# Optimization experiments

Hardware: AMD Instinct MI355X
Metric: run time of the kernel (lower is better)

## Reference

```python
import jax, jax.numpy as jnp
import numpy as np

N_EMBD = 1024
H_DIM = 1024
NB = 16          # blocks resolved by _find_dynamic_num_blocks for all projections
N_MEM = 128
N_FORG = H_DIM - N_MEM
RANK = 64
LOG_DT_INIT = -2.0
EPS = 1.1920929e-07  # torch fp32 finfo eps used by F.rms_norm


def rms_norm(x):
    return x * jax.lax.rsqrt(jnp.mean(jnp.square(x), axis=-1, keepdims=True) + EPS)


def silu(x):
    return x * jax.nn.sigmoid(x)


def blockdiag(x, w):
    # x: [..., nb*bi], w: [nb, bo, bi] -> [..., nb*bo]
    nb, bo, bi = w.shape
    xs = x.reshape(*x.shape[:-1], nb, bi)
    y = jnp.einsum('...ni,noi->...no', xs, w)
    return y.reshape(*x.shape[:-1], nb * bo)


def causal_scan(drive, a):
    # drive: [B,T,D] float32, a: [D] per-channel decay; causal conv with kernel a^t via FFT
    B, T, D = drive.shape
    steps = jnp.arange(T, dtype=jnp.float32)
    kernel = jnp.exp(jnp.log(jnp.maximum(a, 1e-6))[:, None] * steps[None, :])  # [D,T]
    n_fft = 1 << int(2 * T - 1).bit_length()
    df = jnp.fft.rfft(drive.astype(jnp.float32).transpose(0, 2, 1), n=n_fft, axis=-1)
    kf = jnp.fft.rfft(kernel, n=n_fft, axis=-1)
    y = jnp.fft.irfft(df * kf[None], n=n_fft, axis=-1)[..., :T]
    return y.transpose(0, 2, 1).astype(drive.dtype)


def geom_gain(a, K):
    one_minus = 1.0 - a
    safe = jnp.maximum(one_minus, 1e-8)
    return jnp.where(jnp.abs(one_minus) < 1e-6,
                     jnp.full_like(a, float(K)),
                     (1.0 - a ** K) / safe)


def setup_inputs() -> dict:
    key = jax.random.key(0)
    ks = jax.random.split(key, 10)
    s = 0.02
    bi_e, bo_h = N_EMBD // NB, H_DIM // NB
    bi_p = (2 * N_EMBD + H_DIM) // NB
    bo_e = N_EMBD // NB
    return {
        'x': jax.random.normal(ks[0], (4, 4096, N_EMBD), dtype=jnp.float32),
        'active_k': 4,
        'b_seq_w': jax.random.normal(ks[1], (NB, bo_h, bi_e), jnp.float32) * s,
        'b_depth_w': jax.random.normal(ks[2], (NB, bo_h, bi_e), jnp.float32) * s,
        'w_post_w': jax.random.normal(ks[3], (NB, bo_h, bi_p), jnp.float32) * s,
        'w_local_w': jax.random.normal(ks[4], (NB, bo_e, H_DIM // NB), jnp.float32) * s,
        'lr_A': jax.random.normal(ks[5], (N_EMBD, RANK), jnp.float32) * s,
        'lr_B': jax.random.normal(ks[6], (RANK, H_DIM), jnp.float32) * s,
        'log_A_seq': jnp.zeros((H_DIM,), jnp.float32),
        'log_dt_seq': jnp.full((H_DIM,), LOG_DT_INIT, jnp.float32),
        'log_A_depth': jnp.zeros((N_FORG,), jnp.float32),
        'log_dt_depth': jnp.full((N_FORG,), LOG_DT_INIT, jnp.float32),
    }


def reference(x, active_k, b_seq_w, b_depth_w, w_post_w, w_local_w, lr_A, lr_B,
              log_A_seq, log_dt_seq, log_A_depth, log_dt_depth):
    K = int(active_k)
    e = rms_norm(x)
    shifted_e = jnp.pad(e[:, :-1], ((0, 0), (1, 0), (0, 0)))
    a_seq = jnp.exp(-jnp.exp(log_A_seq) * jnp.exp(log_dt_seq))
    h_seq = causal_scan(silu(blockdiag(e, b_seq_w)), a_seq)
    a_forg = jnp.exp(-jnp.exp(log_A_depth) * jnp.exp(log_dt_depth))
    a_depth = jnp.concatenate([jnp.ones((N_MEM,), a_forg.dtype), a_forg], axis=0)
    gain = geom_gain(a_depth, K).astype(x.dtype)
    h_depth = gain * silu(blockdiag(e, b_depth_w))
    h = h_seq + h_depth
    r = silu(blockdiag(jnp.concatenate([rms_norm(h), e, shifted_e], axis=-1), w_post_w))
    out = x + blockdiag(r, w_local_w) + (r @ lr_B.T) @ lr_A.T
    return out
```

## Files before the change

### kernel.cpp

```cpp
#include <hip/hip_runtime.h>

#define B_ 4
#define T_ 4096
#define D_ 1024
#define R_ (B_*T_)
#define CHUNK_ 64
#define NCH_ (T_/CHUNK_)
#define EPS_ 1.1920929e-07f

typedef unsigned short ushort_t;
typedef __attribute__((ext_vector_type(8))) short short8;
typedef __attribute__((ext_vector_type(4))) float f32x4;

__device__ __forceinline__ float silu_f(float v){ return v / (1.0f + __expf(-v)); }

__device__ __forceinline__ ushort_t f2bf(float f){
    unsigned u = __float_as_uint(f);
    unsigned r = u + 0x7fffu + ((u>>16)&1u);
    return (ushort_t)(r>>16);
}
__device__ __forceinline__ float bf2f(ushort_t s){ return __uint_as_float(((unsigned)s)<<16); }

__device__ __forceinline__ f32x4 mfma16(short8 a, short8 b, f32x4 c){
    return __builtin_amdgcn_mfma_f32_16x16x32_bf16(a, b, c, 0, 0, 0);
}

__global__ void prep_k(const float* __restrict__ s0, const float* __restrict__ s1,
                       const float* __restrict__ s2, const float* __restrict__ s3,
                       const float* __restrict__ s4, const float* __restrict__ s5,
                       ushort_t* __restrict__ d0, ushort_t* __restrict__ d1,
                       ushort_t* __restrict__ d2, ushort_t* __restrict__ d3,
                       ushort_t* __restrict__ d4, ushort_t* __restrict__ d5,
                       const float* __restrict__ logA_seq, const float* __restrict__ logdt_seq,
                       const float* __restrict__ logA_dep, const float* __restrict__ logdt_dep,
                       const int* __restrict__ active_k,
                       float* __restrict__ aseq, float* __restrict__ apowC,
                       float* __restrict__ gain, float* __restrict__ apowtab){
    int i = blockIdx.x*256 + threadIdx.x;
    if      (i < 65536)   d0[i] = f2bf(s0[i]);
    else if (i < 131072)  d1[i-65536] = f2bf(s1[i-65536]);
    else if (i < 327680)  d2[i-131072] = f2bf(s2[i-131072]);
    else if (i < 393216)  d3[i-327680] = f2bf(s3[i-327680]);
    else if (i < 458752)  d4[i-393216] = f2bf(s4[i-393216]);
    else if (i < 524288)  d5[i-458752] = f2bf(s5[i-458752]);
    else if (i < 524288 + D_){
        int d = i - 524288;
        float K = (float)(*active_k);
        float a = expf(-expf(logA_seq[d]) * expf(logdt_seq[d]));
        a = fmaxf(a, 1e-6f);
        aseq[d] = a;
        apowC[d] = powf(a, (float)CHUNK_);
        float ap = a;
        for (int s2=0;s2<CHUNK_;++s2){ apowtab[s2*D_ + d] = ap; ap *= a; }
        float g;
        if (d < 128) {
            g = K;
        } else {
            float ad = expf(-expf(logA_dep[d-128]) * expf(logdt_dep[d-128]));
            float om = 1.0f - ad;
            if (fabsf(om) < 1e-6f) g = K;
            else g = (1.0f - powf(ad, K)) / fmaxf(om, 1e-8f);
        }
        gain[d] = g;
    }
}

__global__ __launch_bounds__(256) void rmsbf_k(const float* __restrict__ x, ushort_t* __restrict__ e){
    int row = blockIdx.x;
    int tid = threadIdx.x;
    float4 v = ((const float4*)(x + (size_t)row*D_))[tid];
    float ss = v.x*v.x + v.y*v.y + v.z*v.z + v.w*v.w;
    for (int off=32; off; off>>=1) ss += __shfl_down(ss, off, 64);
    __shared__ float red[4];
    if ((tid&63)==0) red[tid>>6] = ss;
    __syncthreads();
    float tot = red[0]+red[1]+red[2]+red[3];
    float scale = 1.0f / sqrtf(tot*(1.0f/D_) + EPS_);
    ushort4 o;
    o.x = f2bf(v.x*scale); o.y = f2bf(v.y*scale); o.z = f2bf(v.z*scale); o.w = f2bf(v.w*scale);
    ((ushort4*)(e + (size_t)row*D_))[tid] = o;
}

__global__ __launch_bounds__(256) void bd2s_k(const ushort_t* __restrict__ e,
        const ushort_t* __restrict__ wseq, const ushort_t* __restrict__ wdep,
        const float* __restrict__ gain, const float* __restrict__ aseq,
        ushort_t* __restrict__ hsum, float* __restrict__ carry){
    __shared__ __align__(16) ushort_t sd[4][16][72];
    __shared__ __align__(16) ushort_t sh[4][16][72];
    int wave = threadIdx.x>>6, lane = threadIdx.x&63;
    int m = lane&15, quad = lane>>4;
    int orow = lane>>2, oq = lane&3;
    int n = blockIdx.y;
    int chunk0 = blockIdx.x*256 + wave*64;

    short8 bs[2][4], bd[2][4];
    #pragma unroll
    for (int s=0;s<2;++s)
        #pragma unroll
        for (int c=0;c<4;++c){
            bs[s][c] = *(const short8*)(wseq + n*4096 + (c*16+m)*64 + s*32 + quad*8);
            bd[s][c] = *(const short8*)(wdep + n*4096 + (c*16+m)*64 + s*32 + quad*8);
        }
    float g[4];
    #pragma unroll
    for (int c=0;c<4;++c) g[c] = gain[n*64 + c*16 + m];

    float a = aseq[n*64 + lane];
    float hh = 0.f;

    #pragma unroll
    for (int t=0;t<4;++t){
        int r0 = chunk0 + t*16;
        const ushort_t* ab = e + (size_t)(r0+m)*D_ + n*64 + quad*8;
        short8 a0 = *(const short8*)ab;
        short8 a1 = *(const short8*)(ab + 32);
        f32x4 accs[4], accd[4];
        #pragma unroll
        for (int c=0;c<4;++c){
            accs[c]=(f32x4)0.f; accd[c]=(f32x4)0.f;
            accs[c]=mfma16(a0, bs[0][c], accs[c]);
            accd[c]=mfma16(a0, bd[0][c], accd[c]);
            accs[c]=mfma16(a1, bs[1][c], accs[c]);
            accd[c]=mfma16(a1, bd[1][c], accd[c]);
        }
        #pragma unroll
        for (int c=0;c<4;++c)
            #pragma unroll
            for (int r=0;r<4;++r){
                sd[wave][quad*4+r][c*16+m] = f2bf(silu_f(accs[c][r]));
                sh[wave][quad*4+r][c*16+m] = f2bf(g[c]*silu_f(accd[c][r]));
            }
        #pragma unroll
        for (int s=0;s<16;++s){
            hh = fmaf(a, hh, bf2f(sd[wave][s][lane]));
            sd[wave][s][lane] = f2bf(hh + bf2f(sh[wave][s][lane]));
        }
        ushort_t* db = hsum + (size_t)(r0+orow)*D_ + n*64;
        #pragma unroll
        for (int it=0;it<2;++it)
            *(short8*)(db + (it*4+oq)*8) = *(const short8*)&sd[wave][orow][(it*4+oq)*8];
    }
    carry[(size_t)(chunk0>>6)*D_ + n*64 + lane] = hh;
}

__global__ __launch_bounds__(256) void scan2_k(float* __restrict__ carry, const float* __restrict__ apowC){
    int tid = blockIdx.x*256 + threadIdx.x;
    int d = tid & (D_-1);
    int b = tid >> 10;
    float aC = apowC[d];
    float pref = 0.f;
    for (int c=0;c<NCH_;++c){
        size_t idx = (size_t)(b*NCH_+c)*D_ + d;
        float s = carry[idx];
        carry[idx] = pref;
        pref = fmaf(aC, pref, s);
    }
}

__global__ __launch_bounds__(256) void scan3s_k(const ushort_t* __restrict__ hsum,
                                                const float* __restrict__ aseq,
                                                const float* __restrict__ carry,
                                                const float* __restrict__ apowtab,
                                                ushort_t* __restrict__ hn){
    __shared__ float part[4][4];
    __shared__ float scl[8];
    int tid = threadIdx.x;
    int lane = tid & 63, wave = tid >> 6;
    int cg = tid & 127;
    int rp = tid >> 7;
    int d0 = cg*8;
    int row0 = blockIdx.x*8;
    int bc = row0 >> 6;
    int s0 = row0 & 63;

    float a2[8], P[8], apow[8];
    #pragma unroll
    for (int j=0;j<8;++j){
        float aj = aseq[d0+j];
        a2[j] = aj*aj;
        P[j]  = carry[(size_t)bc*D_ + d0 + j];
        apow[j] = apowtab[(size_t)(s0 + rp)*D_ + d0 + j];
    }

    float hf[4][8];
    #pragma unroll
    for (int i=0;i<4;++i){
        int row = row0 + i*2 + rp;
        short8 v = *(const short8*)(hsum + (size_t)row*D_ + d0);
        float ss = 0.f;
        #pragma unroll
        for (int j=0;j<8;++j){
            float f = bf2f((ushort_t)v[j]) + P[j]*apow[j];
            hf[i][j] = f;
            ss += f*f;
            apow[j] *= a2[j];
        }
        for (int off=32; off; off>>=1) ss += __shfl_down(ss, off, 64);
        if (lane==0) part[wave][i] = ss;
    }
    __syncthreads();
    if (tid < 8){
        int r = tid;
        int rr = r & 1, ii = r >> 1;
        float sum = part[rr*2][ii] + part[rr*2+1][ii];
        scl[r] = rsqrtf(sum*(1.0f/D_) + EPS_);
    }
    __syncthreads();
    #pragma unroll
    for (int i=0;i<4;++i){
        int rloc = i*2 + rp;
        float sc = scl[rloc];
        short8 o;
        #pragma unroll
        for (int j=0;j<8;++j) o[j] = (short)f2bf(hf[i][j]*sc);
        *(short8*)(hn + (size_t)(row0 + rloc)*D_ + d0) = o;
    }
}

__global__ __launch_bounds__(256) void post_k(const ushort_t* __restrict__ hn,
                                              const ushort_t* __restrict__ e,
                                              const ushort_t* __restrict__ wpost, ushort_t* __restrict__ rout){
    __shared__ __align__(16) ushort_t st[4][16][72];
    int wave = threadIdx.x>>6, lane = threadIdx.x&63;
    int m = lane&15, quad = lane>>4;
    int orow = lane>>2, oq = lane&3;
    int n = blockIdx.y;
    int row0 = blockIdx.x*128 + wave*32 + m;

    f32x4 acc[2][4];
    #pragma unroll
    for (int t=0;t<2;++t)
        #pragma unroll
        for (int c=0;c<4;++c) acc[t][c]=(f32x4)0.f;

    #pragma unroll 1
    for (int s=0;s<6;++s){
        int g0 = n*192 + s*32;
        short8 bw[4];
        #pragma unroll
        for (int c=0;c<4;++c)
            bw[c] = *(const short8*)(wpost + n*(64*192) + (c*16+m)*192 + s*32 + quad*8);
        #pragma unroll
        for (int t=0;t<2;++t){
            int row = row0 + t*16;
            short8 af;
            if (g0 < 1024){
                af = *(const short8*)(hn + (size_t)row*D_ + g0 + quad*8);
            } else if (g0 < 2048){
                af = *(const short8*)(e + (size_t)row*D_ + (g0-1024) + quad*8);
            } else {
                if ((row & (T_-1)) == 0) af = short8{0,0,0,0,0,0,0,0};
                else af = *(const short8*)(e + (size_t)(row-1)*D_ + (g0-2048) + quad*8);
            }
            #pragma unroll
            for (int c=0;c<4;++c)
                acc[t][c] = mfma16(af, bw[c], acc[t][c]);
        }
    }
    #pragma unroll
    for (int t=0;t<2;++t){
        int r0 = blockIdx.x*128 + wave*32 + t*16;
        #pragma unroll
        for (int c=0;c<4;++c)
            #pragma unroll
            for (int r=0;r<4;++r)
                st[wave][quad*4+r][c*16+m] = f2bf(silu_f(acc[t][c][r]));
        ushort_t* db = rout + (size_t)(r0+orow)*D_ + n*64;
        #pragma unroll
        for (int it=0;it<2;++it)
            *(short8*)(db + (it*4+oq)*8) = *(const short8*)&st[wave][orow][(it*4+oq)*8];
    }
}

__global__ __launch_bounds__(256) void rlow_k(const ushort_t* __restrict__ r, const ushort_t* __restrict__ lrB,
                                              ushort_t* __restrict__ rlow){
    __shared__ __align__(16) float sacc[4][16][68];
    int wave = threadIdx.x>>6, lane = threadIdx.x&63;
    int m = lane&15, quad = lane>>4;
    int r0 = blockIdx.x*16;
    f32x4 acc[4];
    #pragma unroll
    for (int c=0;c<4;++c) acc[c]=(f32x4)0.f;
    const ushort_t* ab = r + (size_t)(r0+m)*D_ + wave*256 + quad*8;
    #pragma unroll
    for (int s=0;s<8;++s){
        short8 a = *(const short8*)(ab + s*32);
        #pragma unroll
        for (int c=0;c<4;++c){
            short8 b = *(const short8*)(lrB + (c*16+m)*1024 + wave*256 + s*32 + quad*8);
            acc[c] = mfma16(a, b, acc[c]);
        }
    }
    #pragma unroll
    for (int c=0;c<4;++c)
        #pragma unroll
        for (int r2=0;r2<4;++r2)
            sacc[wave][quad*4+r2][c*16+m] = acc[c][r2];
    __syncthreads();
    int row  = threadIdx.x>>4;
    int col4 = (threadIdx.x&15)*4;
    float4 v0 = *(const float4*)&sacc[0][row][col4];
    float4 v1 = *(const float4*)&sacc[1][row][col4];
    float4 v2 = *(const float4*)&sacc[2][row][col4];
    float4 v3 = *(const float4*)&sacc[3][row][col4];
    ushort4 o;
    o.x = f2bf(v0.x+v1.x+v2.x+v3.x);
    o.y = f2bf(v0.y+v1.y+v2.y+v3.y);
    o.z = f2bf(v0.z+v1.z+v2.z+v3.z);
    o.w = f2bf(v0.w+v1.w+v2.w+v3.w);
    *(ushort4*)(rlow + (size_t)(r0+row)*64 + col4) = o;
}

__global__ __launch_bounds__(256) void out_k(const float* __restrict__ x, const ushort_t* __restrict__ r,
        const ushort_t* __restrict__ rlow, const ushort_t* __restrict__ wloc, const ushort_t* __restrict__ lrA,
        float* __restrict__ out){
    __shared__ __align__(16) float st[4][16][68];
    int wave = threadIdx.x>>6, lane = threadIdx.x&63;
    int m = lane&15, quad = lane>>4;
    int orow = lane>>2, oq = lane&3;
    int n = blockIdx.y;

    short8 wl[2][4], la[4][2];
    #pragma unroll
    for (int c=0;c<4;++c)
        #pragma unroll
        for (int s=0;s<2;++s){
            wl[s][c] = *(const short8*)(wloc + n*4096 + (c*16+m)*64 + s*32 + quad*8);
            la[c][s] = *(const short8*)(lrA + (size_t)(n*64 + c*16 + m)*64 + s*32 + quad*8);
        }
    #pragma unroll
    for (int t=0;t<2;++t){
        int r0 = blockIdx.x*128 + wave*32 + t*16;
        const float* xb = x + (size_t)(r0+orow)*D_ + n*64;
        float4 xv[4];
        #pragma unroll
        for (int it=0;it<4;++it) xv[it] = *(const float4*)(xb + (it*4+oq)*4);

        const ushort_t* lb = rlow + (size_t)(r0+m)*64 + quad*8;
        short8 al0 = *(const short8*)lb;
        short8 al1 = *(const short8*)(lb + 32);
        const ushort_t* ab = r + (size_t)(r0+m)*D_ + n*64 + quad*8;
        short8 ar0 = *(const short8*)ab;
        short8 ar1 = *(const short8*)(ab + 32);
        f32x4 acc[4];
        #pragma unroll
        for (int c=0;c<4;++c){
            acc[c]=(f32x4)0.f;
            acc[c]=mfma16(al0, la[c][0], acc[c]);
            acc[c]=mfma16(al1, la[c][1], acc[c]);
            acc[c]=mfma16(ar0, wl[0][c], acc[c]);
            acc[c]=mfma16(ar1, wl[1][c], acc[c]);
        }
        #pragma unroll
        for (int c=0;c<4;++c)
            #pragma unroll
            for (int r2=0;r2<4;++r2)
                st[wave][quad*4+r2][c*16+m] = acc[c][r2];
        float* ob = out + (size_t)(r0+orow)*D_ + n*64;
        #pragma unroll
        for (int it=0;it<4;++it){
            float4 v = *(const float4*)&st[wave][orow][(it*4+oq)*4];
            v.x += xv[it].x; v.y += xv[it].y; v.z += xv[it].z; v.w += xv[it].w;
            *(float4*)(ob + (it*4+oq)*4) = v;
        }
    }
}

extern "C" void kernel_launch(void* const* d_in, const int* in_sizes, int n_in,
                              void* d_out, int out_size, void* d_ws, size_t ws_size,
                              hipStream_t stream) {
    const float* x         = (const float*)d_in[0];
    const int*   active_k  = (const int*)  d_in[1];
    const float* b_seq_w   = (const float*)d_in[2];
    const float* b_depth_w = (const float*)d_in[3];
    const float* w_post_w  = (const float*)d_in[4];
    const float* w_local_w = (const float*)d_in[5];
    const float* lr_A      = (const float*)d_in[6];
    const float* lr_B      = (const float*)d_in[7];
    const float* logA_seq  = (const float*)d_in[8];
    const float* logdt_seq = (const float*)d_in[9];
    const float* logA_dep  = (const float*)d_in[10];
    const float* logdt_dep = (const float*)d_in[11];

    float* ws      = (float*)d_ws;
    float* carry   = ws;
    float* aseq    = carry + (size_t)B_*NCH_*D_;
    float* apowC   = aseq + D_;
    float* gain    = apowC + D_;
    float* apowtab = gain + D_;
    ushort_t* ub       = (ushort_t*)(apowtab + (size_t)CHUNK_*D_);
    ushort_t* e_bf     = ub;
    ushort_t* hsum_bf  = e_bf + (size_t)R_*D_;
    ushort_t* hn_bf    = hsum_bf + (size_t)R_*D_;
    ushort_t* r_bf     = hn_bf + (size_t)R_*D_;
    ushort_t* rlow_bf  = r_bf + (size_t)R_*D_;
    ushort_t* wseq_bf  = rlow_bf + (size_t)R_*64;
    ushort_t* wdep_bf  = wseq_bf + 65536;
    ushort_t* wpost_bf = wdep_bf + 65536;
    ushort_t* wloc_bf  = wpost_bf + 196608;
    ushort_t* lrA_bf   = wloc_bf + 65536;
    ushort_t* lrB_bf   = lrA_bf + 65536;

    prep_k<<<(524288 + D_ + 255)/256, 256, 0, stream>>>(
        b_seq_w, b_depth_w, w_post_w, w_local_w, lr_A, lr_B,
        wseq_bf, wdep_bf, wpost_bf, wloc_bf, lrA_bf, lrB_bf,
        logA_seq, logdt_seq, logA_dep, logdt_dep, active_k, aseq, apowC, gain, apowtab);

    rmsbf_k <<<R_, 256, 0, stream>>>(x, e_bf);
    bd2s_k  <<<dim3(R_/256, 16), 256, 0, stream>>>(e_bf, wseq_bf, wdep_bf, gain, aseq,
                                                   hsum_bf, carry);
    scan2_k <<<(B_*D_)/256, 256, 0, stream>>>(carry, apowC);
    scan3s_k<<<R_/8, 256, 0, stream>>>(hsum_bf, aseq, carry, apowtab, hn_bf);
    post_k  <<<dim3(R_/128, 16), 256, 0, stream>>>(hn_bf, e_bf, wpost_bf, r_bf);
    rlow_k  <<<R_/16, 256, 0, stream>>>(r_bf, lrB_bf, rlow_bf);
    out_k   <<<dim3(R_/128, 16), 256, 0, stream>>>(x, r_bf, rlow_bf, wloc_bf, lrA_bf, (float*)d_out);
}
```

Baseline: 271.6 us.

## Parallelize intra-chunk scan with lane shuffles; widen scan2 and out_k grids

The in-chunk linear recurrence in bd2s_k used to run as a serial 16-step loop through shared memory per 16-row tile. It is now a register-level parallel scan: each lane scans its 4 rows locally, and the lanes then combine (decay, offset) pairs across quads with __shfl_up. This also removes the second shared-memory buffer and keeps the scan state in fp32 rather than rounding to bf16 between steps, so numerics change slightly. Separately, scan2_k uses 64-thread blocks and loads all chunk carries into registers up front, and out_k handles one 16-row tile per wave over twice as many blocks, giving more parallelism.

```diff
diff --git a/kernel.cpp b/kernel.cpp
--- a/kernel.cpp
+++ b/kernel.cpp
@@ -85,8 +85,7 @@
         const ushort_t* __restrict__ wseq, const ushort_t* __restrict__ wdep,
         const float* __restrict__ gain, const float* __restrict__ aseq,
         ushort_t* __restrict__ hsum, float* __restrict__ carry){
-    __shared__ __align__(16) ushort_t sd[4][16][72];
-    __shared__ __align__(16) ushort_t sh[4][16][72];
+    __shared__ __align__(16) ushort_t st[4][16][72];
     int wave = threadIdx.x>>6, lane = threadIdx.x&63;
     int m = lane&15, quad = lane>>4;
     int orow = lane>>2, oq = lane&3;
@@ -101,12 +100,16 @@
             bs[s][c] = *(const short8*)(wseq + n*4096 + (c*16+m)*64 + s*32 + quad*8);
             bd[s][c] = *(const short8*)(wdep + n*4096 + (c*16+m)*64 + s*32 + quad*8);
         }
-    float g[4];
-    #pragma unroll
-    for (int c=0;c<4;++c) g[c] = gain[n*64 + c*16 + m];
-
-    float a = aseq[n*64 + lane];
-    float hh = 0.f;
+    float g[4], av[4], a4v[4], C[4];
+    #pragma unroll
+    for (int c=0;c<4;++c){
+        g[c]  = gain[n*64 + c*16 + m];
+        float a = aseq[n*64 + c*16 + m];
+        av[c] = a;
+        float a2 = a*a;
+        a4v[c] = a2*a2;
+        C[c] = 0.f;
+    }
 
     #pragma unroll
     for (int t=0;t<4;++t){
@@ -124,36 +127,59 @@
             accd[c]=mfma16(a1, bd[1][c], accd[c]);
         }
         #pragma unroll
-        for (int c=0;c<4;++c)
-            #pragma unroll
-            for (int r=0;r<4;++r){
-                sd[wave][quad*4+r][c*16+m] = f2bf(silu_f(accs[c][r]));
-                sh[wave][quad*4+r][c*16+m] = f2bf(g[c]*silu_f(accd[c][r]));
-            }
-        #pragma unroll
-        for (int s=0;s<16;++s){
-            hh = fmaf(a, hh, bf2f(sd[wave][s][lane]));
-            sd[wave][s][lane] = f2bf(hh + bf2f(sh[wave][s][lane]));
+        for (int c=0;c<4;++c){
+            float a  = av[c];
+            float d0 = silu_f(accs[c][0]);
+            float d1 = silu_f(accs[c][1]);
+            float d2 = silu_f(accs[c][2]);
+            float d3 = silu_f(accs[c][3]);
+            float p1 = fmaf(a, d0, d1);
+            float p2 = fmaf(a, p1, d2);
+            float p3 = fmaf(a, p2, d3);
+            float M = a4v[c], Bv = p3;
+            float Mp = __shfl_up(M, 16, 64);
+            float Bp = __shfl_up(Bv, 16, 64);
+            if (quad >= 1){ Bv = fmaf(M, Bp, Bv); M *= Mp; }
+            Mp = __shfl_up(M, 32, 64);
+            Bp = __shfl_up(Bv, 32, 64);
+            if (quad >= 2){ Bv = fmaf(M, Bp, Bv); M *= Mp; }
+            float KB = __shfl_up(Bv, 16, 64);
+            float KM = __shfl_up(M, 16, 64);
+            float K  = (quad==0) ? C[c] : fmaf(KM, C[c], KB);
+            float h0 = fmaf(a, K,  d0);
+            float h1 = fmaf(a, h0, d1);
+            float h2 = fmaf(a, h1, d2);
+            float h3 = fmaf(a, h2, d3);
+            float Cn = fmaf(M, C[c], Bv);
+            C[c] = __shfl(Cn, 48 + m, 64);
+            st[wave][quad*4+0][c*16+m] = f2bf(h0 + g[c]*silu_f(accd[c][0]));
+            st[wave][quad*4+1][c*16+m] = f2bf(h1 + g[c]*silu_f(accd[c][1]));
+            st[wave][quad*4+2][c*16+m] = f2bf(h2 + g[c]*silu_f(accd[c][2]));
+            st[wave][quad*4+3][c*16+m] = f2bf(h3 + g[c]*silu_f(accd[c][3]));
         }
         ushort_t* db = hsum + (size_t)(r0+orow)*D_ + n*64;
         #pragma unroll
         for (int it=0;it<2;++it)
-            *(short8*)(db + (it*4+oq)*8) = *(const short8*)&sd[wave][orow][(it*4+oq)*8];
-    }
-    carry[(size_t)(chunk0>>6)*D_ + n*64 + lane] = hh;
-}
-
-__global__ __launch_bounds__(256) void scan2_k(float* __restrict__ carry, const float* __restrict__ apowC){
-    int tid = blockIdx.x*256 + threadIdx.x;
+            *(short8*)(db + (it*4+oq)*8) = *(const short8*)&st[wave][orow][(it*4+oq)*8];
+    }
+    float Cv = (quad==0) ? C[0] : (quad==1) ? C[1] : (quad==2) ? C[2] : C[3];
+    carry[(size_t)(chunk0>>6)*D_ + n*64 + lane] = Cv;
+}
+
+__global__ __launch_bounds__(64) void scan2_k(float* __restrict__ carry, const float* __restrict__ apowC){
+    int tid = blockIdx.x*64 + threadIdx.x;
     int d = tid & (D_-1);
     int b = tid >> 10;
     float aC = apowC[d];
+    float s[NCH_];
+    #pragma unroll
+    for (int c=0;c<NCH_;++c) s[c] = carry[(size_t)(b*NCH_+c)*D_ + d];
     float pref = 0.f;
+    #pragma unroll
     for (int c=0;c<NCH_;++c){
-        size_t idx = (size_t)(b*NCH_+c)*D_ + d;
-        float s = carry[idx];
-        carry[idx] = pref;
-        pref = fmaf(aC, pref, s);
+        float cur = s[c];
+        carry[(size_t)(b*NCH_+c)*D_ + d] = pref;
+        pref = fmaf(aC, pref, cur);
     }
 }
 
@@ -319,6 +345,7 @@
     int m = lane&15, quad = lane>>4;
     int orow = lane>>2, oq = lane&3;
     int n = blockIdx.y;
+    int r0 = blockIdx.x*64 + wave*16;
 
     short8 wl[2][4], la[4][2];
     #pragma unroll
@@ -328,41 +355,37 @@
             wl[s][c] = *(const short8*)(wloc + n*4096 + (c*16+m)*64 + s*32 + quad*8);
             la[c][s] = *(const short8*)(lrA + (size_t)(n*64 + c*16 + m)*64 + s*32 + quad*8);
         }
-    #pragma unroll
-    for (int t=0;t<2;++t){
-        int r0 = blockIdx.x*128 + wave*32 + t*16;
-        const float* xb = x + (size_t)(r0+orow)*D_ + n*64;
-        float4 xv[4];
-        #pragma unroll
-        for (int it=0;it<4;++it) xv[it] = *(const float4*)(xb + (it*4+oq)*4);
-
-        const ushort_t* lb = rlow + (size_t)(r0+m)*64 + quad*8;
-        short8 al0 = *(const short8*)lb;
-        short8 al1 = *(const short8*)(lb + 32);
-        const ushort_t* ab = r + (size_t)(r0+m)*D_ + n*64 + quad*8;
-        short8 ar0 = *(const short8*)ab;
-        short8 ar1 = *(const short8*)(ab + 32);
-        f32x4 acc[4];
-        #pragma unroll
-        for (int c=0;c<4;++c){
-            acc[c]=(f32x4)0.f;
-            acc[c]=mfma16(al0, la[c][0], acc[c]);
-            acc[c]=mfma16(al1, la[c][1], acc[c]);
-            acc[c]=mfma16(ar0, wl[0][c], acc[c]);
-            acc[c]=mfma16(ar1, wl[1][c], acc[c]);
-        }
-        #pragma unroll
-        for (int c=0;c<4;++c)
-            #pragma unroll
-            for (int r2=0;r2<4;++r2)
-                st[wave][quad*4+r2][c*16+m] = acc[c][r2];
-        float* ob = out + (size_t)(r0+orow)*D_ + n*64;
-        #pragma unroll
-        for (int it=0;it<4;++it){
-            float4 v = *(const float4*)&st[wave][orow][(it*4+oq)*4];
-            v.x += xv[it].x; v.y += xv[it].y; v.z += xv[it].z; v.w += xv[it].w;
-            *(float4*)(ob + (it*4+oq)*4) = v;
-        }
+    const float* xb = x + (size_t)(r0+orow)*D_ + n*64;
+    float4 xv[4];
+    #pragma unroll
+    for (int it=0;it<4;++it) xv[it] = *(const float4*)(xb + (it*4+oq)*4);
+
+    const ushort_t* lb = rlow + (size_t)(r0+m)*64 + quad*8;
+    short8 al0 = *(const short8*)lb;
+    short8 al1 = *(const short8*)(lb + 32);
+    const ushort_t* ab = r + (size_t)(r0+m)*D_ + n*64 + quad*8;
+    short8 ar0 = *(const short8*)ab;
+    short8 ar1 = *(const short8*)(ab + 32);
+    f32x4 acc[4];
+    #pragma unroll
+    for (int c=0;c<4;++c){
+        acc[c]=(f32x4)0.f;
+        acc[c]=mfma16(al0, la[c][0], acc[c]);
+        acc[c]=mfma16(al1, la[c][1], acc[c]);
+        acc[c]=mfma16(ar0, wl[0][c], acc[c]);
+        acc[c]=mfma16(ar1, wl[1][c], acc[c]);
+    }
+    #pragma unroll
+    for (int c=0;c<4;++c)
+        #pragma unroll
+        for (int r2=0;r2<4;++r2)
+            st[wave][quad*4+r2][c*16+m] = acc[c][r2];
+    float* ob = out + (size_t)(r0+orow)*D_ + n*64;
+    #pragma unroll
+    for (int it=0;it<4;++it){
+        float4 v = *(const float4*)&st[wave][orow][(it*4+oq)*4];
+        v.x += xv[it].x; v.y += xv[it].y; v.z += xv[it].z; v.w += xv[it].w;
+        *(float4*)(ob + (it*4+oq)*4) = v;
     }
 }
 
@@ -409,9 +432,9 @@
     rmsbf_k <<<R_, 256, 0, stream>>>(x, e_bf);
     bd2s_k  <<<dim3(R_/256, 16), 256, 0, stream>>>(e_bf, wseq_bf, wdep_bf, gain, aseq,
                                                    hsum_bf, carry);
-    scan2_k <<<(B_*D_)/256, 256, 0, stream>>>(carry, apowC);
+    scan2_k <<<(B_*D_)/64, 64, 0, stream>>>(carry, apowC);
     scan3s_k<<<R_/8, 256, 0, stream>>>(hsum_bf, aseq, carry, apowtab, hn_bf);
     post_k  <<<dim3(R_/128, 16), 256, 0, stream>>>(hn_bf, e_bf, wpost_bf, r_bf);
     rlow_k  <<<R_/16, 256, 0, stream>>>(r_bf, lrB_bf, rlow_bf);
-    out_k   <<<dim3(R_/128, 16), 256, 0, stream>>>(x, r_bf, rlow_bf, wloc_bf, lrA_bf, (float*)d_out);
-}
+    out_k   <<<dim3(R_/64, 16), 256, 0, stream>>>(x, r_bf, rlow_bf, wloc_bf, lrA_bf, (float*)d_out);
+}
```

Result: slower. 279.4 us (+2.9%).
